# Optimization experiments

Measured on AMD Instinct MI355X. Metric: run time of the kernel, lower is better.

Reference implementation:

```python
import jax, jax.numpy as jnp
import numpy as np

E = 4      # num_ensemble
DIN = 256  # input_dim
D = 256    # d_model (output_dim)
B = 16
T = 1024
LN_EPS = 1e-5


def setup_inputs() -> dict:
    key = jax.random.key(0)
    ks = jax.random.split(key, 14)
    s = 0.02
    x = jax.random.normal(ks[0], (B, T, DIN), dtype=jnp.float32)
    in_proj_w = s * jax.random.normal(ks[1], (3, E, DIN, D), dtype=jnp.float32)
    in_proj_b = jnp.zeros((3, E, D), dtype=jnp.float32)
    mid_w = s * jax.random.normal(ks[2], (2, E, D, D), dtype=jnp.float32)
    mid_b = jnp.zeros((2, E, D), dtype=jnp.float32)
    ff_w1 = s * jax.random.normal(ks[3], (E, D, D), dtype=jnp.float32)
    ff_b1 = jnp.zeros((E, D), dtype=jnp.float32)
    ff_w2 = s * jax.random.normal(ks[4], (E, D, D), dtype=jnp.float32)
    ff_b2 = jnp.zeros((E, D), dtype=jnp.float32)
    ln_w = jnp.ones((E, D), dtype=jnp.float32)
    ln_b = jnp.zeros((E, D), dtype=jnp.float32)
    # LRU initializer (r_min=0.9, r_max=0.999)
    r_min, r_max = 0.9, 0.999
    u1 = jax.random.uniform(ks[5], (E, D), dtype=jnp.float32)
    u2 = jax.random.uniform(ks[6], (E, D), dtype=jnp.float32)
    nu_log = jnp.log(-0.5 * jnp.log(u1 * (r_max ** 2 - r_min ** 2) + r_min ** 2))
    theta_log = jnp.log(u2 * 2.0 * np.pi)
    # |lambda|^2 = exp(-2*exp(nu_log))
    gamma_log = jnp.log(jnp.sqrt(1.0 - jnp.exp(-2.0 * jnp.exp(nu_log))))
    params_log = jnp.stack([nu_log, theta_log, gamma_log], axis=0)  # (3,E,D)
    return {"x": x, "in_proj_w": in_proj_w, "in_proj_b": in_proj_b,
            "params_log": params_log, "mid_w": mid_w, "mid_b": mid_b,
            "ff_w1": ff_w1, "ff_b1": ff_b1, "ff_w2": ff_w2, "ff_b2": ff_b2,
            "ln_w": ln_w, "ln_b": ln_b}


def _forward(x, in_proj_w, in_proj_b, params_log, mid_w, mid_b,
             ff_w1, ff_b1, ff_w2, ff_b2, ln_w, ln_b):
    # in_proj: 3 ensemble linears -> u: (3, E, B, T, D)
    u = jnp.einsum('bti,keio->kebto', x, in_proj_w) + in_proj_b[:, :, None, None, :]
    input_real, input_imag, o = u[0], u[1], u[2]

    params = jnp.exp(params_log)           # (3,E,D)
    nu, theta, gamma = params[0], params[1], params[2]
    mag = jnp.exp(-nu)
    f_real = mag * jnp.cos(theta)          # (E,D)
    f_imag = mag * jnp.sin(theta)

    ir = gamma[:, None, None, :] * input_real  # (E,B,T,D)
    ii = gamma[:, None, None, :] * input_imag

    # complex linear recurrence h_t = f * h_{t-1} + u_t over time axis
    fr = f_real[:, None, :]                # (E,1,D) broadcast over B
    fi = f_imag[:, None, :]
    ir_t = jnp.moveaxis(ir, 2, 0)          # (T,E,B,D)
    ii_t = jnp.moveaxis(ii, 2, 0)

    def step(carry, ut):
        hr, hi = carry
        ur, ui = ut
        hr2 = fr * hr - fi * hi + ur
        hi2 = fr * hi + fi * hr + ui
        return (hr2, hi2), (hr2, hi2)

    h0 = (jnp.zeros((E, B, D), x.dtype), jnp.zeros((E, B, D), x.dtype))
    (hr_last, hi_last), (out_r_t, out_i_t) = jax.lax.scan(step, h0, (ir_t, ii_t))
    output_real = jnp.moveaxis(out_r_t, 0, 2)  # (E,B,T,D)
    output_imag = jnp.moveaxis(out_i_t, 0, 2)

    # hidden packing: (1, B, 2*E*D) with ensemble blocks concatenated, real then imag
    hr_pack = jnp.transpose(hr_last, (1, 0, 2)).reshape(B, E * D)
    hi_pack = jnp.transpose(hi_last, (1, 0, 2)).reshape(B, E * D)
    hidden = jnp.concatenate([hr_pack, hi_pack], axis=-1)[None]  # (1,B,2ED)

    # middle_proj: 2 ensemble linears applied to (real, imag)
    stacked = jnp.stack([output_real, output_imag], axis=0)  # (2,E,B,T,D)
    mid = jnp.einsum('kebtd,kedo->kebto', stacked, mid_w) + mid_b[:, :, None, None, :]
    out = mid[0] - mid[1] + o                                # (E,B,T,D)

    # EnsemblePositionWiseFeedForward (dropout=0 -> identity)
    h1 = jax.nn.gelu(jnp.einsum('ebtd,edo->ebto', out, ff_w1)
                     + ff_b1[:, None, None, :], approximate=False)
    h2 = jnp.einsum('ebtd,edo->ebto', h1, ff_w2) + ff_b2[:, None, None, :] + out
    # LayerNorm over joint (E, D) dims for each (b, t)
    mean = jnp.mean(h2, axis=(0, 3), keepdims=True)
    var = jnp.var(h2, axis=(0, 3), keepdims=True)
    out_ln = (h2 - mean) / jnp.sqrt(var + LN_EPS)
    out_ln = out_ln * ln_w[:, None, None, :] + ln_b[:, None, None, :]
    return out_ln, hidden


def reference(x, in_proj_w, in_proj_b, params_log, mid_w, mid_b,
              ff_w1, ff_b1, ff_w2, ff_b2, ln_w, ln_b):
    return _forward(x, in_proj_w, in_proj_b, params_log, mid_w, mid_b,
                    ff_w1, ff_b1, ff_w2, ff_b2, ln_w, ln_b)
```

## Files before the change

### kernel.cpp

```cpp
#include <hip/hip_runtime.h>
#include <stdint.h>

#define BT_ 16384
#define TT  1024
#define CHUNKS 32
#define CLEN   32
#define LANES  16384

typedef __bf16 bf16x8 __attribute__((ext_vector_type(8)));
typedef float  f32x4  __attribute__((ext_vector_type(4)));
typedef unsigned int u32x4 __attribute__((ext_vector_type(4)));
typedef unsigned short u16;

__device__ __forceinline__ float b2f(u16 s){
    union { float f; unsigned int u; } c; c.u = ((unsigned int)s) << 16; return c.f;
}
__device__ __forceinline__ u16 f2b(float f){
    union { float f; unsigned int u; } c; c.f = f;
    unsigned int u = c.u;
    return (u16)((u + 0x7fffu + ((u >> 16) & 1u)) >> 16);
}

__device__ __forceinline__ void gload_lds16(const u16* g, u16* lds){
    __builtin_amdgcn_global_load_lds(
        (const __attribute__((address_space(1))) void*)g,
        (__attribute__((address_space(3))) void*)lds, 16, 0, 0);
}

__global__ __launch_bounds__(256) void conv_k(const float* __restrict__ x, u16* __restrict__ xc)
{
    long i = (long)blockIdx.x * 256 + threadIdx.x;
    xc[i] = f2b(x[i]);
}

__global__ __launch_bounds__(256) void prep_w(
    const float* __restrict__ ipw, const float* __restrict__ mw,
    const float* __restrict__ fw1, const float* __restrict__ fw2,
    u16* __restrict__ d_ipw, u16* __restrict__ d_mw,
    u16* __restrict__ d_fw1, u16* __restrict__ d_fw2)
{
    __shared__ u16 tile[64][72];
    int blk = blockIdx.x;
    int w = blk >> 4, t = blk & 15;
    int tr = (t >> 2) * 64;
    int tc = (t & 3) * 64;
    const float* src; u16* dst; int ostride; float sign = 1.f;
    if (w < 12)      { src = ipw + (size_t)w * 65536; dst = d_ipw + (size_t)w * 65536; ostride = 256; }
    else if (w < 20) { int u = w - 12, c = u >> 2, e = u & 3;
                       src = mw + (size_t)u * 65536;
                       dst = d_mw + (size_t)e * 131072 + c * 256; ostride = 512;
                       if (c) sign = -1.f; }
    else if (w < 24) { int e = w - 20; src = fw1 + (size_t)e * 65536; dst = d_fw1 + (size_t)e * 65536; ostride = 256; }
    else             { int e = w - 24; src = fw2 + (size_t)e * 65536; dst = d_fw2 + (size_t)e * 65536; ostride = 256; }

    int q = threadIdx.x;
    int r = q >> 2, cb = (q & 3) * 16;
#pragma unroll
    for (int j = 0; j < 4; j++) {
        int col = cb + j * 4;
        const float4 v = *reinterpret_cast<const float4*>(src + (size_t)(tr + r) * 256 + tc + col);
        tile[r][col + 0] = f2b(v.x * sign);
        tile[r][col + 1] = f2b(v.y * sign);
        tile[r][col + 2] = f2b(v.z * sign);
        tile[r][col + 3] = f2b(v.w * sign);
    }
    __syncthreads();
    int ol = q >> 2, ib = (q & 3) * 16;
    union { u16 s[8]; u32x4 v; } p0, p1;
#pragma unroll
    for (int k = 0; k < 8; k++) { p0.s[k] = tile[ib + k][ol]; p1.s[k] = tile[ib + 8 + k][ol]; }
    u16* drow = dst + (size_t)(tc + ol) * ostride + tr + ib;
    *reinterpret_cast<u32x4*>(drow)     = p0.v;
    *reinterpret_cast<u32x4*>(drow + 8) = p1.v;
}

__global__ __launch_bounds__(256, 4) void gemm_k(
    const u16* __restrict__ A0, const u16* __restrict__ B0,
    const float* __restrict__ biasf, const u16* __restrict__ aux,
    const float* __restrict__ gamlogf, u16* __restrict__ out0,
    u16* __restrict__ out1, int K, int mode)
{
    __shared__ __align__(16) u16 Bs[64 * 256];

    int tid  = threadIdx.x;
    int wave = tid >> 6, lane = tid & 63;
    int quad = lane >> 4, l16 = lane & 15;
    int m0 = blockIdx.x * 128, n0 = blockIdx.y * 64;
    int z = blockIdx.z;
    int e, k3 = 0;
    const u16* A;
    const u16* Bm;
    if (mode == 1) { k3 = z >> 2; e = z & 3; A = A0; }
    else           { e = z; A = A0 + (size_t)e * BT_ * K; }
    Bm = B0 + (size_t)(mode == 1 ? z : e) * 256 * K;

    f32x4 acc[2][4];
#pragma unroll
    for (int i = 0; i < 2; i++)
#pragma unroll
        for (int j = 0; j < 4; j++) acc[i][j] = (f32x4){0.f, 0.f, 0.f, 0.f};

    int srow = lane >> 5, schunk = lane & 31;
    int nhalf = K >> 8;

    for (int kh = 0; kh < nhalf; kh++) {
        if (kh) __syncthreads();
#pragma unroll
        for (int i = 0; i < 8; i++) {
            int row = wave * 16 + i * 2 + srow;
            int c = schunk ^ (row & 7);
            gload_lds16(Bm + (size_t)(n0 + row) * K + kh * 256 + c * 8,
                        &Bs[(wave * 16 + i * 2) * 256]);
        }
        __syncthreads();

        const u16* Arow0 = A + (size_t)(m0 + wave * 32 + l16) * K + kh * 256 + quad * 8;
        const u16* Arow1 = Arow0 + (size_t)16 * K;

        bf16x8 a0c, a1c, a0n, a1n;
        { union { u32x4 v; bf16x8 b; } u; u.v = *reinterpret_cast<const u32x4*>(Arow0); a0c = u.b; }
        { union { u32x4 v; bf16x8 b; } u; u.v = *reinterpret_cast<const u32x4*>(Arow1); a1c = u.b; }
#pragma unroll
        for (int kt = 0; kt < 8; kt++) {
            if (kt < 7) {
                union { u32x4 v; bf16x8 b; } u;
                u.v = *reinterpret_cast<const u32x4*>(Arow0 + (kt + 1) * 32); a0n = u.b;
                u.v = *reinterpret_cast<const u32x4*>(Arow1 + (kt + 1) * 32); a1n = u.b;
            }
#pragma unroll
            for (int nf = 0; nf < 4; nf++) {
                int row = nf * 16 + l16;
                int c = (kt * 4 + quad) ^ (row & 7);
                union { u32x4 v; bf16x8 b; } u;
                u.v = *reinterpret_cast<const u32x4*>(&Bs[row * 256 + c * 8]);
                acc[0][nf] = __builtin_amdgcn_mfma_f32_16x16x32_bf16(a0c, u.b, acc[0][nf], 0, 0, 0);
                acc[1][nf] = __builtin_amdgcn_mfma_f32_16x16x32_bf16(a1c, u.b, acc[1][nf], 0, 0, 0);
            }
            a0c = a0n; a1c = a1n;
        }
    }

    float bias_nf[4], gam_nf[4];
#pragma unroll
    for (int nf = 0; nf < 4; nf++) {
        int col = n0 + nf * 16 + l16;
        if (mode == 1) {
            bias_nf[nf] = biasf[z * 256 + col];
            gam_nf[nf] = (k3 < 2) ? expf(gamlogf[2048 + e * 256 + col]) : 1.f;
        } else if (mode == 2) {
            bias_nf[nf] = biasf[e * 256 + col] - biasf[1024 + e * 256 + col];
        } else {
            bias_nf[nf] = biasf[e * 256 + col];
        }
    }

#pragma unroll
    for (int mf = 0; mf < 2; mf++) {
#pragma unroll
        for (int nf = 0; nf < 4; nf++) {
            int col = n0 + nf * 16 + l16;
#pragma unroll
            for (int r = 0; r < 4; r++) {
                int row = m0 + wave * 32 + mf * 16 + quad * 4 + r;
                float v = acc[mf][nf][r] + bias_nf[nf];
                size_t pidx = ((size_t)e * BT_ + row) * 256 + col;
                if (mode == 1) {
                    if (k3 < 2) {
                        out0[((size_t)(e * BT_ + row) * 2 + k3) * 256 + col] = f2b(v * gam_nf[nf]);
                    } else {
                        out1[pidx] = f2b(v);
                    }
                } else if (mode == 2) {
                    out0[pidx] = f2b(v + b2f(aux[pidx]));
                } else if (mode == 3) {
                    v = 0.5f * v * (1.0f + erff(v * 0.70710678118654752f));
                    out0[pidx] = f2b(v);
                } else {
                    out0[pidx] = f2b(v + b2f(aux[pidx]));
                }
            }
        }
    }
}

__global__ __launch_bounds__(256) void scan_a(const u16* __restrict__ u,
    const float* __restrict__ plog, float2* __restrict__ carry)
{
    int l2 = blockIdx.x * 256 + threadIdx.x;
    int chunk = blockIdx.y;
    int dd = (l2 & 127) * 2, b = (l2 >> 7) & 15, e = l2 >> 11;
    float nu0 = expf(plog[e * 256 + dd]),        nu1 = expf(plog[e * 256 + dd + 1]);
    float th0 = expf(plog[1024 + e * 256 + dd]), th1 = expf(plog[1024 + e * 256 + dd + 1]);
    float m0 = expf(-nu0), m1 = expf(-nu1);
    float fr0 = m0 * cosf(th0), fi0 = m0 * sinf(th0);
    float fr1 = m1 * cosf(th1), fi1 = m1 * sinf(th1);
    size_t base = ((size_t)e * BT_ + b * TT) * 512 + (size_t)chunk * CLEN * 512 + dd;
    float hr0 = 0.f, hi0 = 0.f, hr1 = 0.f, hi1 = 0.f;
    for (int t = 0; t < CLEN; t++) {
        unsigned int wr = *reinterpret_cast<const unsigned int*>(u + base);
        unsigned int wi = *reinterpret_cast<const unsigned int*>(u + base + 256);
        float ur0 = b2f((u16)wr), ur1 = b2f((u16)(wr >> 16));
        float ui0 = b2f((u16)wi), ui1 = b2f((u16)(wi >> 16));
        float a0 = fr0 * hr0 - fi0 * hi0 + ur0;
        float b0 = fr0 * hi0 + fi0 * hr0 + ui0;
        float a1 = fr1 * hr1 - fi1 * hi1 + ur1;
        float b1 = fr1 * hi1 + fi1 * hr1 + ui1;
        hr0 = a0; hi0 = b0; hr1 = a1; hi1 = b1;
        base += 512;
    }
    size_t ci = (size_t)chunk * LANES + (size_t)e * 4096 + b * 256 + dd;
    *reinterpret_cast<float4*>(&carry[ci]) = make_float4(hr0, hi0, hr1, hi1);
}

__global__ __launch_bounds__(256) void scan_b(const float* __restrict__ plog,
                                              float2* __restrict__ carry)
{
    int l = blockIdx.x * 256 + threadIdx.x;
    int d = l & 255, e = l >> 12;
    float nu = expf(plog[e * 256 + d]);
    float th = expf(plog[1024 + e * 256 + d]);
    float magL = expf(-nu * (float)CLEN);
    float ang = th * (float)CLEN;
    float frL = magL * cosf(ang), fiL = magL * sinf(ang);
    float gr = 0.f, gi = 0.f;
    for (int j = 0; j < CHUNKS; j++) {
        float2 c = carry[(size_t)j * LANES + l];
        carry[(size_t)j * LANES + l] = make_float2(gr, gi);
        float gr2 = frL * gr - fiL * gi + c.x;
        float gi2 = frL * gi + fiL * gr + c.y;
        gr = gr2; gi = gi2;
    }
}

__global__ __launch_bounds__(256) void scan_c(u16* __restrict__ u,
    const float* __restrict__ plog, const float2* __restrict__ carry,
    float* __restrict__ outh)
{
    int l2 = blockIdx.x * 256 + threadIdx.x;
    int chunk = blockIdx.y;
    int dd = (l2 & 127) * 2, b = (l2 >> 7) & 15, e = l2 >> 11;
    float nu0 = expf(plog[e * 256 + dd]),        nu1 = expf(plog[e * 256 + dd + 1]);
    float th0 = expf(plog[1024 + e * 256 + dd]), th1 = expf(plog[1024 + e * 256 + dd + 1]);
    float m0 = expf(-nu0), m1 = expf(-nu1);
    float fr0 = m0 * cosf(th0), fi0 = m0 * sinf(th0);
    float fr1 = m1 * cosf(th1), fi1 = m1 * sinf(th1);
    size_t base = ((size_t)e * BT_ + b * TT) * 512 + (size_t)chunk * CLEN * 512 + dd;
    size_t ci = (size_t)chunk * LANES + (size_t)e * 4096 + b * 256 + dd;
    float4 c0 = *reinterpret_cast<const float4*>(&carry[ci]);
    float hr0 = c0.x, hi0 = c0.y, hr1 = c0.z, hi1 = c0.w;
    for (int t = 0; t < CLEN; t++) {
        unsigned int wr = *reinterpret_cast<const unsigned int*>(u + base);
        unsigned int wi = *reinterpret_cast<const unsigned int*>(u + base + 256);
        float ur0 = b2f((u16)wr), ur1 = b2f((u16)(wr >> 16));
        float ui0 = b2f((u16)wi), ui1 = b2f((u16)(wi >> 16));
        float a0 = fr0 * hr0 - fi0 * hi0 + ur0;
        float b0 = fr0 * hi0 + fi0 * hr0 + ui0;
        float a1 = fr1 * hr1 - fi1 * hi1 + ur1;
        float b1 = fr1 * hi1 + fi1 * hr1 + ui1;
        hr0 = a0; hi0 = b0; hr1 = a1; hi1 = b1;
        *reinterpret_cast<unsigned int*>(u + base) =
            (unsigned int)f2b(hr0) | ((unsigned int)f2b(hr1) << 16);
        *reinterpret_cast<unsigned int*>(u + base + 256) =
            (unsigned int)f2b(hi0) | ((unsigned int)f2b(hi1) << 16);
        base += 512;
    }
    if (chunk == CHUNKS - 1) {
        float* oh = outh + (size_t)4 * BT_ * 256;
        *reinterpret_cast<float2*>(&oh[b * 2048 + e * 256 + dd])        = make_float2(hr0, hr1);
        *reinterpret_cast<float2*>(&oh[b * 2048 + 1024 + e * 256 + dd]) = make_float2(hi0, hi1);
    }
}

__global__ __launch_bounds__(256) void ln_k(const u16* __restrict__ h2,
    const float* __restrict__ lnw, const float* __restrict__ lnb,
    float* __restrict__ out)
{
    int r = blockIdx.x;
    int d = threadIdx.x;
    float v[4]; float s1 = 0.f, s2 = 0.f;
#pragma unroll
    for (int e = 0; e < 4; e++) {
        float x = b2f(h2[((size_t)e * BT_ + r) * 256 + d]);
        v[e] = x; s1 += x; s2 += x * x;
    }
#pragma unroll
    for (int off = 32; off; off >>= 1) {
        s1 += __shfl_down(s1, off, 64);
        s2 += __shfl_down(s2, off, 64);
    }
    __shared__ float sm[8];
    int wave = threadIdx.x >> 6, lane = threadIdx.x & 63;
    if (lane == 0) { sm[wave] = s1; sm[4 + wave] = s2; }
    __syncthreads();
    float S1 = sm[0] + sm[1] + sm[2] + sm[3];
    float S2 = sm[4] + sm[5] + sm[6] + sm[7];
    float mean = S1 * (1.0f / 1024.0f);
    float var = S2 * (1.0f / 1024.0f) - mean * mean;
    float rstd = rsqrtf(var + 1e-5f);
#pragma unroll
    for (int e = 0; e < 4; e++) {
        float o = (v[e] - mean) * rstd * lnw[e * 256 + d] + lnb[e * 256 + d];
        out[((size_t)e * BT_ + r) * 256 + d] = o;
    }
}

extern "C" void kernel_launch(void* const* d_in, const int* in_sizes, int n_in,
                              void* d_out, int out_size, void* d_ws, size_t ws_size,
                              hipStream_t stream)
{
    const float* x    = (const float*)d_in[0];
    const float* ipw  = (const float*)d_in[1];
    const float* ipb  = (const float*)d_in[2];
    const float* plog = (const float*)d_in[3];
    const float* mw   = (const float*)d_in[4];
    const float* mb   = (const float*)d_in[5];
    const float* fw1  = (const float*)d_in[6];
    const float* fb1  = (const float*)d_in[7];
    const float* fw2  = (const float*)d_in[8];
    const float* fb2  = (const float*)d_in[9];
    const float* lnw  = (const float*)d_in[10];
    const float* lnb  = (const float*)d_in[11];
    float* out = (float*)d_out;

    u16* W = (u16*)d_ws;
    u16* buf_u    = W;
    u16* buf_out  = W + (size_t)33554432;
    u16* xc       = W + (size_t)33554432;
    float2* carry = (float2*)(W + (size_t)37748736);
    u16* buf_mw_t = W + (size_t)50331648;
    u16* c_ipw_t  = W + (size_t)50855936;
    u16* c_fw1_t  = W + (size_t)51642368;
    u16* c_fw2_t  = W + (size_t)51904512;
    u16* scratch  = (u16*)d_out;

    conv_k<<<16384, 256, 0, stream>>>(x, xc);
    prep_w<<<448, 256, 0, stream>>>(ipw, mw, fw1, fw2, c_ipw_t, buf_mw_t, c_fw1_t, c_fw2_t);
    gemm_k<<<dim3(128, 4, 12), 256, 0, stream>>>(xc, c_ipw_t, ipb, nullptr, plog, buf_u, scratch, 256, 1);
    scan_a<<<dim3(32, CHUNKS), 256, 0, stream>>>(buf_u, plog, carry);
    scan_b<<<64, 256, 0, stream>>>(plog, carry);
    scan_c<<<dim3(32, CHUNKS), 256, 0, stream>>>(buf_u, plog, carry, out);
    gemm_k<<<dim3(128, 4, 4), 256, 0, stream>>>(buf_u, buf_mw_t, mb, scratch, nullptr, buf_out, nullptr, 512, 2);
    gemm_k<<<dim3(128, 4, 4), 256, 0, stream>>>(buf_out, c_fw1_t, fb1, nullptr, nullptr, scratch, nullptr, 256, 3);
    gemm_k<<<dim3(128, 4, 4), 256, 0, stream>>>(scratch, c_fw2_t, fb2, buf_out, nullptr, buf_u, nullptr, 256, 4);
    ln_k<<<16384, 256, 0, stream>>>(buf_u, lnw, lnb, out);
}
```

Baseline: 359.6 us.

## Vectorize conversion, stage GEMM epilogue through LDS for 16-byte stores

The fp32-to-bf16 conversion kernel now handles eight elements per thread with float4 loads and a single 16-byte store, launching an eighth as many blocks. In the GEMM, the A fragments for the K-slice are prefetched two steps ahead into register arrays, and the launch bounds now request 5 blocks per CU instead of 4. The epilogue writes accumulators to shared memory and then emits coalesced 16-byte bf16 stores, with the residual also read as 16-byte vectors, in place of scattered 2-byte stores. This targets store and load inefficiency, at the cost of an extra barrier and LDS round trip, plus register pressure from the larger prefetch arrays under the tighter occupancy bound.

```diff
diff --git a/kernel.cpp b/kernel.cpp
--- a/kernel.cpp
+++ b/kernel.cpp
@@ -29,8 +29,13 @@
 
 __global__ __launch_bounds__(256) void conv_k(const float* __restrict__ x, u16* __restrict__ xc)
 {
-    long i = (long)blockIdx.x * 256 + threadIdx.x;
-    xc[i] = f2b(x[i]);
+    long i = ((long)blockIdx.x * 256 + threadIdx.x) * 8;
+    float4 v0 = *reinterpret_cast<const float4*>(x + i);
+    float4 v1 = *reinterpret_cast<const float4*>(x + i + 4);
+    union { u16 s[8]; u32x4 v; } p;
+    p.s[0] = f2b(v0.x); p.s[1] = f2b(v0.y); p.s[2] = f2b(v0.z); p.s[3] = f2b(v0.w);
+    p.s[4] = f2b(v1.x); p.s[5] = f2b(v1.y); p.s[6] = f2b(v1.z); p.s[7] = f2b(v1.w);
+    *reinterpret_cast<u32x4*>(xc + i) = p.v;
 }
 
 __global__ __launch_bounds__(256) void prep_w(
@@ -74,7 +79,7 @@
     *reinterpret_cast<u32x4*>(drow + 8) = p1.v;
 }
 
-__global__ __launch_bounds__(256, 4) void gemm_k(
+__global__ __launch_bounds__(256, 5) void gemm_k(
     const u16* __restrict__ A0, const u16* __restrict__ B0,
     const float* __restrict__ biasf, const u16* __restrict__ aux,
     const float* __restrict__ gamlogf, u16* __restrict__ out0,
@@ -117,15 +122,19 @@
         const u16* Arow0 = A + (size_t)(m0 + wave * 32 + l16) * K + kh * 256 + quad * 8;
         const u16* Arow1 = Arow0 + (size_t)16 * K;
 
-        bf16x8 a0c, a1c, a0n, a1n;
-        { union { u32x4 v; bf16x8 b; } u; u.v = *reinterpret_cast<const u32x4*>(Arow0); a0c = u.b; }
-        { union { u32x4 v; bf16x8 b; } u; u.v = *reinterpret_cast<const u32x4*>(Arow1); a1c = u.b; }
+        bf16x8 a0[8], a1[8];
+#pragma unroll
+        for (int p = 0; p < 2; p++) {
+            union { u32x4 v; bf16x8 b; } u0, u1;
+            u0.v = *reinterpret_cast<const u32x4*>(Arow0 + p * 32); a0[p] = u0.b;
+            u1.v = *reinterpret_cast<const u32x4*>(Arow1 + p * 32); a1[p] = u1.b;
+        }
 #pragma unroll
         for (int kt = 0; kt < 8; kt++) {
-            if (kt < 7) {
-                union { u32x4 v; bf16x8 b; } u;
-                u.v = *reinterpret_cast<const u32x4*>(Arow0 + (kt + 1) * 32); a0n = u.b;
-                u.v = *reinterpret_cast<const u32x4*>(Arow1 + (kt + 1) * 32); a1n = u.b;
+            if (kt < 6) {
+                union { u32x4 v; bf16x8 b; } u0, u1;
+                u0.v = *reinterpret_cast<const u32x4*>(Arow0 + (kt + 2) * 32); a0[kt + 2] = u0.b;
+                u1.v = *reinterpret_cast<const u32x4*>(Arow1 + (kt + 2) * 32); a1[kt + 2] = u1.b;
             }
 #pragma unroll
             for (int nf = 0; nf < 4; nf++) {
@@ -133,10 +142,9 @@
                 int c = (kt * 4 + quad) ^ (row & 7);
                 union { u32x4 v; bf16x8 b; } u;
                 u.v = *reinterpret_cast<const u32x4*>(&Bs[row * 256 + c * 8]);
-                acc[0][nf] = __builtin_amdgcn_mfma_f32_16x16x32_bf16(a0c, u.b, acc[0][nf], 0, 0, 0);
-                acc[1][nf] = __builtin_amdgcn_mfma_f32_16x16x32_bf16(a1c, u.b, acc[1][nf], 0, 0, 0);
+                acc[0][nf] = __builtin_amdgcn_mfma_f32_16x16x32_bf16(a0[kt], u.b, acc[0][nf], 0, 0, 0);
+                acc[1][nf] = __builtin_amdgcn_mfma_f32_16x16x32_bf16(a1[kt], u.b, acc[1][nf], 0, 0, 0);
             }
-            a0c = a0n; a1c = a1n;
         }
     }
 
@@ -154,32 +162,48 @@
         }
     }
 
-#pragma unroll
-    for (int mf = 0; mf < 2; mf++) {
-#pragma unroll
-        for (int nf = 0; nf < 4; nf++) {
-            int col = n0 + nf * 16 + l16;
+    __syncthreads();
+    float* fs = reinterpret_cast<float*>(Bs) + wave * 2048;
+#pragma unroll
+    for (int mf = 0; mf < 2; mf++)
+#pragma unroll
+        for (int nf = 0; nf < 4; nf++)
 #pragma unroll
             for (int r = 0; r < 4; r++) {
-                int row = m0 + wave * 32 + mf * 16 + quad * 4 + r;
                 float v = acc[mf][nf][r] + bias_nf[nf];
-                size_t pidx = ((size_t)e * BT_ + row) * 256 + col;
-                if (mode == 1) {
-                    if (k3 < 2) {
-                        out0[((size_t)(e * BT_ + row) * 2 + k3) * 256 + col] = f2b(v * gam_nf[nf]);
-                    } else {
-                        out1[pidx] = f2b(v);
-                    }
-                } else if (mode == 2) {
-                    out0[pidx] = f2b(v + b2f(aux[pidx]));
-                } else if (mode == 3) {
-                    v = 0.5f * v * (1.0f + erff(v * 0.70710678118654752f));
-                    out0[pidx] = f2b(v);
-                } else {
-                    out0[pidx] = f2b(v + b2f(aux[pidx]));
-                }
+                if (mode == 1) v *= gam_nf[nf];
+                if (mode == 3) v = 0.5f * v * (1.0f + erff(v * 0.70710678118654752f));
+                fs[(mf * 16 + quad * 4 + r) * 64 + nf * 16 + l16] = v;
             }
-        }
+
+    int rr = lane >> 3, ch = lane & 7;
+#pragma unroll
+    for (int i = 0; i < 4; i++) {
+        int rl = i * 8 + rr;
+        int grow = m0 + wave * 32 + rl;
+        const f32x4* sp = reinterpret_cast<const f32x4*>(fs + rl * 64 + ch * 8);
+        f32x4 v0 = sp[0], v1 = sp[1];
+        float w[8] = { v0[0], v0[1], v0[2], v0[3], v1[0], v1[1], v1[2], v1[3] };
+        u16* dstp;
+        if (mode == 1) {
+            if (k3 < 2) dstp = out0 + (((size_t)(e * BT_ + grow)) * 2 + k3) * 256 + n0 + ch * 8;
+            else        dstp = out1 + ((size_t)e * BT_ + grow) * 256 + n0 + ch * 8;
+        } else {
+            dstp = out0 + ((size_t)e * BT_ + grow) * 256 + n0 + ch * 8;
+        }
+        if (mode == 2 || mode == 4) {
+            const u16* ap = aux + ((size_t)e * BT_ + grow) * 256 + n0 + ch * 8;
+            u32x4 av = *reinterpret_cast<const u32x4*>(ap);
+#pragma unroll
+            for (int j = 0; j < 4; j++) {
+                w[2 * j]     += b2f((u16)(av[j] & 0xffffu));
+                w[2 * j + 1] += b2f((u16)(av[j] >> 16));
+            }
+        }
+        union { u16 s[8]; u32x4 v; } p;
+#pragma unroll
+        for (int j = 0; j < 8; j++) p.s[j] = f2b(w[j]);
+        *reinterpret_cast<u32x4*>(dstp) = p.v;
     }
 }
 
@@ -333,7 +357,7 @@
     u16* c_fw2_t  = W + (size_t)51904512;
     u16* scratch  = (u16*)d_out;
 
-    conv_k<<<16384, 256, 0, stream>>>(x, xc);
+    conv_k<<<2048, 256, 0, stream>>>(x, xc);
     prep_w<<<448, 256, 0, stream>>>(ipw, mw, fw1, fw2, c_ipw_t, buf_mw_t, c_fw1_t, c_fw2_t);
     gemm_k<<<dim3(128, 4, 12), 256, 0, stream>>>(xc, c_ipw_t, ipb, nullptr, plog, buf_u, scratch, 256, 1);
     scan_a<<<dim3(32, CHUNKS), 256, 0, stream>>>(buf_u, plog, carry);
```

After: 343.2 us. -4.5%, faster.
